# Performance work log

Hardware: AMD Instinct MI355X
Metric: run time of the kernel (lower is better)

## Reference

```python
import jax, jax.numpy as jnp
import numpy as np

SEQLEN = 4096
DIM = 4096
HIDDEN = 11008  # multiple_of=256 rounding of int(2*16384/3)


def setup_inputs() -> dict:
    key = jax.random.key(0)
    k1, k2, k3, k4 = jax.random.split(key, 4)
    scale = 1.0 / np.sqrt(DIM)
    return {
        "x": jax.random.normal(k1, (SEQLEN, DIM), dtype=jnp.float32),
        "weight_1": jax.random.normal(k2, (DIM, HIDDEN), dtype=jnp.float32) * scale,
        "weight_2": jax.random.normal(k3, (HIDDEN, DIM), dtype=jnp.float32) * (1.0 / np.sqrt(HIDDEN)),
        "weight_3": jax.random.normal(k4, (DIM, HIDDEN), dtype=jnp.float32) * scale,
    }


def reference(x, weight_1, weight_2, weight_3):
    # The torch module decomposes these GEMMs into 128x128 tile loops, but
    # the math is exactly the standard SwiGLU FFN:
    #   out = (silu(x @ W1) * (x @ W3)) @ W2
    gate = x @ weight_1                      # [S, H]
    up = x @ weight_3                        # [S, H]
    h = jax.nn.silu(gate) * up               # [S, H]
    return h @ weight_2                      # [S, D]
```

## Files before the change

kernel.cpp:

```cpp
#include <hip/hip_runtime.h>
#include <stdint.h>
#include <stddef.h>

#define AS1 __attribute__((address_space(1)))
#define AS3 __attribute__((address_space(3)))

typedef __attribute__((ext_vector_type(8))) short bf16x8;
typedef __attribute__((ext_vector_type(4))) float f32x4;

static constexpr int S = 4096, D = 4096, HID = 11008;

__device__ __forceinline__ unsigned short f2bf(float f) {
  unsigned u = __float_as_uint(f);
  u += 0x7FFFu + ((u >> 16) & 1u);
  return (unsigned short)(u >> 16);
}

__device__ __forceinline__ void async16(const void* gsrc, void* ldst) {
  __builtin_amdgcn_global_load_lds((AS1 void*)const_cast<void*>(gsrc),
                                   (AS3 void*)ldst, 16, 0, 0);
}

__global__ __launch_bounds__(256) void k_cvt_bf16(const float* __restrict__ src,
                                                  unsigned short* __restrict__ dst) {
  int i = blockIdx.x * 256 + threadIdx.x;
  const float4* s = (const float4*)src;
  float4 a = s[2 * i];
  float4 b = s[2 * i + 1];
  union { unsigned short h[8]; uint4 v; } r;
  r.h[0] = f2bf(a.x); r.h[1] = f2bf(a.y); r.h[2] = f2bf(a.z); r.h[3] = f2bf(a.w);
  r.h[4] = f2bf(b.x); r.h[5] = f2bf(b.y); r.h[6] = f2bf(b.z); r.h[7] = f2bf(b.w);
  ((uint4*)dst)[i] = r.v;
}

__global__ __launch_bounds__(256) void k_tcvt(const float* __restrict__ src,
                                              unsigned short* __restrict__ dst,
                                              int R, int C) {
  __shared__ float tile[64][65];
  const int tid = threadIdx.x;
  const int c0 = blockIdx.x * 64;
  const int r0 = blockIdx.y * 64;
#pragma unroll
  for (int it = 0; it < 16; ++it) {
    int f = it * 256 + tid;
    int r = f >> 6, c = f & 63;
    tile[r][c] = src[(size_t)(r0 + r) * C + (c0 + c)];
  }
  __syncthreads();
#pragma unroll
  for (int it = 0; it < 8; ++it) {
    int f = it * 512 + tid * 2;
    int cc = f >> 6, rr = f & 63;
    unsigned p0 = f2bf(tile[rr][cc]);
    unsigned p1 = f2bf(tile[rr + 1][cc]);
    *(unsigned*)(dst + (size_t)(c0 + cc) * R + (r0 + rr)) = p0 | (p1 << 16);
  }
}

__global__ __launch_bounds__(256, 2) void gemm_gateup(
    const unsigned short* __restrict__ A,
    const unsigned short* __restrict__ B1,
    const unsigned short* __restrict__ B3,
    unsigned short* __restrict__ Hout) {
  __shared__ __align__(16) unsigned short sA[128 * 32];
  __shared__ __align__(16) unsigned short sB1[64 * 32];
  __shared__ __align__(16) unsigned short sB3[64 * 32];

  const int tid = threadIdx.x;
  const int wave = tid >> 6, lane = tid & 63;
  const int wy = wave >> 1, wx = wave & 1;
  const int lm = lane & 15, lq = lane >> 4;
  const int m0 = blockIdx.x * 128;
  const int n0 = blockIdx.y * 64;

  const int ci0 = wave * 64 + lane;
  const int rA0 = ci0 >> 2, cA0 = (ci0 & 3) * 8;
  const int ci1 = ci0 + 256;
  const int rA1 = ci1 >> 2, cA1 = (ci1 & 3) * 8;

  const unsigned short* pA0 = A + (size_t)(m0 + rA0) * D + cA0;
  const unsigned short* pA1 = A + (size_t)(m0 + rA1) * D + cA1;
  const unsigned short* pB1 = B1 + (size_t)(n0 + rA0) * D + cA0;
  const unsigned short* pB3 = B3 + (size_t)(n0 + rA0) * D + cA0;
  unsigned short* lA0 = sA + wave * 512;
  unsigned short* lA1 = sA + 2048 + wave * 512;
  unsigned short* lB1 = sB1 + wave * 512;
  unsigned short* lB3 = sB3 + wave * 512;

  f32x4 zero = {0.f, 0.f, 0.f, 0.f};
  f32x4 accg[4][2], accu[4][2];
#pragma unroll
  for (int i = 0; i < 4; ++i)
#pragma unroll
    for (int j = 0; j < 2; ++j) { accg[i][j] = zero; accu[i][j] = zero; }

  for (int kt = 0; kt < D / 32; ++kt) {
    __syncthreads();
    async16(pA0, lA0);
    async16(pA1, lA1);
    async16(pB1, lB1);
    async16(pB3, lB3);
    pA0 += 32; pA1 += 32; pB1 += 32; pB3 += 32;
    __syncthreads();

    bf16x8 af[4];
#pragma unroll
    for (int i = 0; i < 4; ++i)
      af[i] = *(const bf16x8*)(sA + (wy * 64 + i * 16 + lm) * 32 + lq * 8);
#pragma unroll
    for (int j = 0; j < 2; ++j) {
      bf16x8 b1f = *(const bf16x8*)(sB1 + (wx * 32 + j * 16 + lm) * 32 + lq * 8);
      bf16x8 b3f = *(const bf16x8*)(sB3 + (wx * 32 + j * 16 + lm) * 32 + lq * 8);
#pragma unroll
      for (int i = 0; i < 4; ++i) {
        accg[i][j] = __builtin_amdgcn_mfma_f32_16x16x32_bf16(af[i], b1f, accg[i][j], 0, 0, 0);
        accu[i][j] = __builtin_amdgcn_mfma_f32_16x16x32_bf16(af[i], b3f, accu[i][j], 0, 0, 0);
      }
    }
  }

#pragma unroll
  for (int i = 0; i < 4; ++i)
#pragma unroll
    for (int j = 0; j < 2; ++j) {
      int col = n0 + wx * 32 + j * 16 + lm;
#pragma unroll
      for (int r = 0; r < 4; ++r) {
        int row = m0 + wy * 64 + i * 16 + lq * 4 + r;
        float g = accg[i][j][r];
        float u = accu[i][j][r];
        float hv = (g / (1.0f + __expf(-g))) * u;
        Hout[(size_t)row * HID + col] = f2bf(hv);
      }
    }
}

__global__ __launch_bounds__(256, 2) void gemm_out(
    const unsigned short* __restrict__ A,
    const unsigned short* __restrict__ B,
    float* __restrict__ C) {
  __shared__ __align__(16) unsigned short sA[128 * 32];
  __shared__ __align__(16) unsigned short sB[128 * 32];

  const int tid = threadIdx.x;
  const int wave = tid >> 6, lane = tid & 63;
  const int wy = wave >> 1, wx = wave & 1;
  const int lm = lane & 15, lq = lane >> 4;
  const int m0 = blockIdx.x * 128;
  const int n0 = blockIdx.y * 128;

  const int ci0 = wave * 64 + lane;
  const int r0 = ci0 >> 2, c0 = (ci0 & 3) * 8;
  const int ci1 = ci0 + 256;
  const int r1 = ci1 >> 2, c1 = (ci1 & 3) * 8;

  const unsigned short* pA0 = A + (size_t)(m0 + r0) * HID + c0;
  const unsigned short* pA1 = A + (size_t)(m0 + r1) * HID + c1;
  const unsigned short* pB0 = B + (size_t)(n0 + r0) * HID + c0;
  const unsigned short* pB1 = B + (size_t)(n0 + r1) * HID + c1;
  unsigned short* lA0 = sA + wave * 512;
  unsigned short* lA1 = sA + 2048 + wave * 512;
  unsigned short* lB0 = sB + wave * 512;
  unsigned short* lB1 = sB + 2048 + wave * 512;

  f32x4 zero = {0.f, 0.f, 0.f, 0.f};
  f32x4 acc[4][4];
#pragma unroll
  for (int i = 0; i < 4; ++i)
#pragma unroll
    for (int j = 0; j < 4; ++j) acc[i][j] = zero;

  for (int kt = 0; kt < HID / 32; ++kt) {
    __syncthreads();
    async16(pA0, lA0);
    async16(pA1, lA1);
    async16(pB0, lB0);
    async16(pB1, lB1);
    pA0 += 32; pA1 += 32; pB0 += 32; pB1 += 32;
    __syncthreads();

    bf16x8 af[4];
#pragma unroll
    for (int i = 0; i < 4; ++i)
      af[i] = *(const bf16x8*)(sA + (wy * 64 + i * 16 + lm) * 32 + lq * 8);
#pragma unroll
    for (int j = 0; j < 4; ++j) {
      bf16x8 bfj = *(const bf16x8*)(sB + (wx * 64 + j * 16 + lm) * 32 + lq * 8);
#pragma unroll
      for (int i = 0; i < 4; ++i)
        acc[i][j] = __builtin_amdgcn_mfma_f32_16x16x32_bf16(af[i], bfj, acc[i][j], 0, 0, 0);
    }
  }

#pragma unroll
  for (int i = 0; i < 4; ++i)
#pragma unroll
    for (int j = 0; j < 4; ++j) {
      int col = n0 + wx * 64 + j * 16 + lm;
#pragma unroll
      for (int r = 0; r < 4; ++r) {
        int row = m0 + wy * 64 + i * 16 + lq * 4 + r;
        C[(size_t)row * D + col] = acc[i][j][r];
      }
    }
}

extern "C" void kernel_launch(void* const* d_in, const int* in_sizes, int n_in,
                              void* d_out, int out_size, void* d_ws, size_t ws_size,
                              hipStream_t stream) {
  const float* x  = (const float*)d_in[0];
  const float* w1 = (const float*)d_in[1];
  const float* w2 = (const float*)d_in[2];
  const float* w3 = (const float*)d_in[3];
  float* out = (float*)d_out;

  char* ws = (char*)d_ws;
  unsigned short* xb   = (unsigned short*)(ws);
  unsigned short* w1t  = (unsigned short*)(ws + (size_t)33554432);
  unsigned short* w3t  = (unsigned short*)(ws + (size_t)123731968);
  unsigned short* hbuf = (unsigned short*)(ws + (size_t)213909504);
  unsigned short* w2t  = w1t;

  k_cvt_bf16<<<dim3((S * D) / 8 / 256), 256, 0, stream>>>(x, xb);
  k_tcvt<<<dim3(HID / 64, D / 64), 256, 0, stream>>>(w1, w1t, D, HID);
  k_tcvt<<<dim3(HID / 64, D / 64), 256, 0, stream>>>(w3, w3t, D, HID);
  gemm_gateup<<<dim3(S / 128, HID / 64), 256, 0, stream>>>(xb, w1t, w3t, hbuf);
  k_tcvt<<<dim3(D / 64, HID / 64), 256, 0, stream>>>(w2, w2t, HID, D);
  gemm_out<<<dim3(S / 128, D / 128), 256, 0, stream>>>(hbuf, w2t, out);
}
```

Measured before the change: 1.822 ms.

## Rewrite both GEMMs with larger tiles, 4-stage async LDS pipeline and swizzle

Both GEMM kernels move to 512-thread blocks with 256x128 (gate/up) and 256x256 (out) tiles. A 4-deep ring of global-to-LDS async loads is driven by explicit vmcnt waits and split barriers. The LDS layout is XOR-swizzled to avoid bank conflicts, and block indices are remapped across XCDs. MFMA phases get raised wave priority. The aim is to hide global load latency and raise arithmetic intensity, at the cost of 128KB LDS per block and heavy register pressure from the larger accumulator sets.

```diff
diff --git a/kernel.cpp b/kernel.cpp
--- a/kernel.cpp
+++ b/kernel.cpp
@@ -57,76 +57,124 @@
   }
 }
 
-__global__ __launch_bounds__(256, 2) void gemm_gateup(
+
+__global__ __launch_bounds__(512, 2) void gemm_gateup(
     const unsigned short* __restrict__ A,
     const unsigned short* __restrict__ B1,
     const unsigned short* __restrict__ B3,
     unsigned short* __restrict__ Hout) {
-  __shared__ __align__(16) unsigned short sA[128 * 32];
-  __shared__ __align__(16) unsigned short sB1[64 * 32];
-  __shared__ __align__(16) unsigned short sB3[64 * 32];
-
+  __shared__ __align__(16) unsigned short sL[65536];
+  constexpr int NT = D / 32;
   const int tid = threadIdx.x;
   const int wave = tid >> 6, lane = tid & 63;
-  const int wy = wave >> 1, wx = wave & 1;
+  const int wy = wave >> 2, wx = wave & 3;
   const int lm = lane & 15, lq = lane >> 4;
-  const int m0 = blockIdx.x * 128;
-  const int n0 = blockIdx.y * 64;
-
-  const int ci0 = wave * 64 + lane;
-  const int rA0 = ci0 >> 2, cA0 = (ci0 & 3) * 8;
-  const int ci1 = ci0 + 256;
-  const int rA1 = ci1 >> 2, cA1 = (ci1 & 3) * 8;
-
-  const unsigned short* pA0 = A + (size_t)(m0 + rA0) * D + cA0;
-  const unsigned short* pA1 = A + (size_t)(m0 + rA1) * D + cA1;
-  const unsigned short* pB1 = B1 + (size_t)(n0 + rA0) * D + cA0;
-  const unsigned short* pB3 = B3 + (size_t)(n0 + rA0) * D + cA0;
-  unsigned short* lA0 = sA + wave * 512;
-  unsigned short* lA1 = sA + 2048 + wave * 512;
-  unsigned short* lB1 = sB1 + wave * 512;
-  unsigned short* lB3 = sB3 + wave * 512;
+
+  const int q = (int)gridDim.x >> 3;
+  const int wg = (blockIdx.x & 7) * q + (blockIdx.x >> 3);
+  const int m0 = (wg / (HID / 128)) * 256;
+  const int n0 = (wg % (HID / 128)) * 128;
+
+  const int h = lm >> 1;
+  const int sw = ((((lm & 1) << 2) | lq) ^ h);
+  const int aBase  = (wy * 64 + h) * 64 + sw * 8;
+  const int b1Base = 8192  + (wx * 16 + h) * 64 + sw * 8;
+  const int b3Base = 12288 + (wx * 16 + h) * 64 + sw * 8;
+
+  const int p0 = tid >> 3, s0 = tid & 7;
+  const int u0 = s0 ^ (p0 & 7);
+  const int rr0 = 2 * p0 + (u0 >> 2);
+  const int kc0 = (u0 & 3) * 8;
+
+  const unsigned short* pA0 = A  + (size_t)(m0 + rr0) * D + kc0;
+  const unsigned short* pA1 = pA0 + (size_t)128 * D;
+  const unsigned short* pB1 = B1 + (size_t)(n0 + rr0) * D + kc0;
+  const unsigned short* pB3 = B3 + (size_t)(n0 + rr0) * D + kc0;
 
   f32x4 zero = {0.f, 0.f, 0.f, 0.f};
-  f32x4 accg[4][2], accu[4][2];
-#pragma unroll
-  for (int i = 0; i < 4; ++i)
+  f32x4 accg[8][2], accu[8][2];
+#pragma unroll
+  for (int i = 0; i < 8; ++i)
 #pragma unroll
     for (int j = 0; j < 2; ++j) { accg[i][j] = zero; accu[i][j] = zero; }
 
-  for (int kt = 0; kt < D / 32; ++kt) {
-    __syncthreads();
-    async16(pA0, lA0);
-    async16(pA1, lA1);
-    async16(pB1, lB1);
-    async16(pB3, lB3);
+#pragma unroll
+  for (int x = 0; x < 3; ++x) {
+    const int nso = x * 16384;
+    async16(pA0, sL + nso + wave * 512);
+    async16(pA1, sL + nso + 4096 + wave * 512);
+    async16(pB1, sL + nso + 8192 + wave * 512);
+    async16(pB3, sL + nso + 12288 + wave * 512);
     pA0 += 32; pA1 += 32; pB1 += 32; pB3 += 32;
-    __syncthreads();
-
-    bf16x8 af[4];
+  }
+  asm volatile("s_waitcnt vmcnt(8)" ::: "memory");
+  __builtin_amdgcn_s_barrier();
+
+  for (int t = 0; t < NT; ++t) {
+    const int so  = (t & 3) * 16384;
+    const int nso = ((t + 3) & 3) * 16384;
+    const bool st = (t + 3 < NT);
+    bf16x8 b1f[2], b3f[2], af[4];
+#pragma unroll
+    for (int j = 0; j < 2; ++j) {
+      b1f[j] = *(const bf16x8*)(sL + so + b1Base + j * 512);
+      b3f[j] = *(const bf16x8*)(sL + so + b3Base + j * 512);
+    }
 #pragma unroll
     for (int i = 0; i < 4; ++i)
-      af[i] = *(const bf16x8*)(sA + (wy * 64 + i * 16 + lm) * 32 + lq * 8);
+      af[i] = *(const bf16x8*)(sL + so + aBase + i * 512);
+    if (st) {
+      async16(pA0, sL + nso + wave * 512);
+      async16(pA1, sL + nso + 4096 + wave * 512);
+      pA0 += 32; pA1 += 32;
+    }
+    __builtin_amdgcn_s_barrier();
+    asm volatile("s_waitcnt lgkmcnt(0)" ::: "memory");
+    __builtin_amdgcn_sched_barrier(0);
+    __builtin_amdgcn_s_setprio(1);
+#pragma unroll
+    for (int j = 0; j < 2; ++j)
+#pragma unroll
+      for (int i = 0; i < 4; ++i) {
+        accg[i][j] = __builtin_amdgcn_mfma_f32_16x16x32_bf16(af[i], b1f[j], accg[i][j], 0, 0, 0);
+        accu[i][j] = __builtin_amdgcn_mfma_f32_16x16x32_bf16(af[i], b3f[j], accu[i][j], 0, 0, 0);
+      }
+    __builtin_amdgcn_s_setprio(0);
+    __builtin_amdgcn_s_barrier();
+#pragma unroll
+    for (int i = 0; i < 4; ++i)
+      af[i] = *(const bf16x8*)(sL + so + aBase + (4 + i) * 512);
+    if (st) {
+      async16(pB1, sL + nso + 8192 + wave * 512);
+      async16(pB3, sL + nso + 12288 + wave * 512);
+      pB1 += 32; pB3 += 32;
+    }
+    __builtin_amdgcn_s_barrier();
+    asm volatile("s_waitcnt lgkmcnt(0)" ::: "memory");
+    __builtin_amdgcn_sched_barrier(0);
+    __builtin_amdgcn_s_setprio(1);
+#pragma unroll
+    for (int j = 0; j < 2; ++j)
+#pragma unroll
+      for (int i = 0; i < 4; ++i) {
+        accg[4 + i][j] = __builtin_amdgcn_mfma_f32_16x16x32_bf16(af[i], b1f[j], accg[4 + i][j], 0, 0, 0);
+        accu[4 + i][j] = __builtin_amdgcn_mfma_f32_16x16x32_bf16(af[i], b3f[j], accu[4 + i][j], 0, 0, 0);
+      }
+    __builtin_amdgcn_s_setprio(0);
+    if (t + 3 < NT)      asm volatile("s_waitcnt vmcnt(8)" ::: "memory");
+    else if (t + 2 < NT) asm volatile("s_waitcnt vmcnt(4)" ::: "memory");
+    else if (t + 1 < NT) asm volatile("s_waitcnt vmcnt(0)" ::: "memory");
+    __builtin_amdgcn_s_barrier();
+  }
+
+#pragma unroll
+  for (int i = 0; i < 8; ++i)
 #pragma unroll
     for (int j = 0; j < 2; ++j) {
-      bf16x8 b1f = *(const bf16x8*)(sB1 + (wx * 32 + j * 16 + lm) * 32 + lq * 8);
-      bf16x8 b3f = *(const bf16x8*)(sB3 + (wx * 32 + j * 16 + lm) * 32 + lq * 8);
-#pragma unroll
-      for (int i = 0; i < 4; ++i) {
-        accg[i][j] = __builtin_amdgcn_mfma_f32_16x16x32_bf16(af[i], b1f, accg[i][j], 0, 0, 0);
-        accu[i][j] = __builtin_amdgcn_mfma_f32_16x16x32_bf16(af[i], b3f, accu[i][j], 0, 0, 0);
-      }
-    }
-  }
-
-#pragma unroll
-  for (int i = 0; i < 4; ++i)
-#pragma unroll
-    for (int j = 0; j < 2; ++j) {
-      int col = n0 + wx * 32 + j * 16 + lm;
+      const int col = n0 + wx * 32 + j * 16 + lm;
 #pragma unroll
       for (int r = 0; r < 4; ++r) {
-        int row = m0 + wy * 64 + i * 16 + lq * 4 + r;
+        const int row = m0 + wy * 128 + i * 16 + lq * 4 + r;
         float g = accg[i][j][r];
         float u = accu[i][j][r];
         float hv = (g / (1.0f + __expf(-g))) * u;
@@ -135,71 +183,115 @@
     }
 }
 
-__global__ __launch_bounds__(256, 2) void gemm_out(
+__global__ __launch_bounds__(512, 2) void gemm_out(
     const unsigned short* __restrict__ A,
     const unsigned short* __restrict__ B,
     float* __restrict__ C) {
-  __shared__ __align__(16) unsigned short sA[128 * 32];
-  __shared__ __align__(16) unsigned short sB[128 * 32];
-
+  __shared__ __align__(16) unsigned short sL[65536];
+  constexpr int NT = HID / 32;
   const int tid = threadIdx.x;
   const int wave = tid >> 6, lane = tid & 63;
-  const int wy = wave >> 1, wx = wave & 1;
+  const int wy = wave >> 2, wx = wave & 3;
   const int lm = lane & 15, lq = lane >> 4;
-  const int m0 = blockIdx.x * 128;
-  const int n0 = blockIdx.y * 128;
-
-  const int ci0 = wave * 64 + lane;
-  const int r0 = ci0 >> 2, c0 = (ci0 & 3) * 8;
-  const int ci1 = ci0 + 256;
-  const int r1 = ci1 >> 2, c1 = (ci1 & 3) * 8;
-
-  const unsigned short* pA0 = A + (size_t)(m0 + r0) * HID + c0;
-  const unsigned short* pA1 = A + (size_t)(m0 + r1) * HID + c1;
-  const unsigned short* pB0 = B + (size_t)(n0 + r0) * HID + c0;
-  const unsigned short* pB1 = B + (size_t)(n0 + r1) * HID + c1;
-  unsigned short* lA0 = sA + wave * 512;
-  unsigned short* lA1 = sA + 2048 + wave * 512;
-  unsigned short* lB0 = sB + wave * 512;
-  unsigned short* lB1 = sB + 2048 + wave * 512;
+
+  const int q = (int)gridDim.x >> 3;
+  const int wg = (blockIdx.x & 7) * q + (blockIdx.x >> 3);
+  const int m0 = (wg >> 4) * 256;
+  const int n0 = (wg & 15) * 256;
+
+  const int h = lm >> 1;
+  const int sw = ((((lm & 1) << 2) | lq) ^ h);
+  const int aBase = (wy * 64 + h) * 64 + sw * 8;
+  const int bBase = 8192 + (wx * 32 + h) * 64 + sw * 8;
+
+  const int p0 = tid >> 3, s0 = tid & 7;
+  const int u0 = s0 ^ (p0 & 7);
+  const int rr0 = 2 * p0 + (u0 >> 2);
+  const int kc0 = (u0 & 3) * 8;
+
+  const unsigned short* pA0 = A + (size_t)(m0 + rr0) * HID + kc0;
+  const unsigned short* pA1 = pA0 + (size_t)128 * HID;
+  const unsigned short* pB0 = B + (size_t)(n0 + rr0) * HID + kc0;
+  const unsigned short* pB1 = pB0 + (size_t)128 * HID;
 
   f32x4 zero = {0.f, 0.f, 0.f, 0.f};
-  f32x4 acc[4][4];
-#pragma unroll
-  for (int i = 0; i < 4; ++i)
+  f32x4 acc[8][4];
+#pragma unroll
+  for (int i = 0; i < 8; ++i)
 #pragma unroll
     for (int j = 0; j < 4; ++j) acc[i][j] = zero;
 
-  for (int kt = 0; kt < HID / 32; ++kt) {
-    __syncthreads();
-    async16(pA0, lA0);
-    async16(pA1, lA1);
-    async16(pB0, lB0);
-    async16(pB1, lB1);
+#pragma unroll
+  for (int x = 0; x < 3; ++x) {
+    const int nso = x * 16384;
+    async16(pA0, sL + nso + wave * 512);
+    async16(pA1, sL + nso + 4096 + wave * 512);
+    async16(pB0, sL + nso + 8192 + wave * 512);
+    async16(pB1, sL + nso + 12288 + wave * 512);
     pA0 += 32; pA1 += 32; pB0 += 32; pB1 += 32;
-    __syncthreads();
-
-    bf16x8 af[4];
+  }
+  asm volatile("s_waitcnt vmcnt(8)" ::: "memory");
+  __builtin_amdgcn_s_barrier();
+
+  for (int t = 0; t < NT; ++t) {
+    const int so  = (t & 3) * 16384;
+    const int nso = ((t + 3) & 3) * 16384;
+    const bool st = (t + 3 < NT);
+    bf16x8 bf[4], af[4];
+#pragma unroll
+    for (int j = 0; j < 4; ++j)
+      bf[j] = *(const bf16x8*)(sL + so + bBase + j * 512);
 #pragma unroll
     for (int i = 0; i < 4; ++i)
-      af[i] = *(const bf16x8*)(sA + (wy * 64 + i * 16 + lm) * 32 + lq * 8);
+      af[i] = *(const bf16x8*)(sL + so + aBase + i * 512);
+    if (st) {
+      async16(pA0, sL + nso + wave * 512);
+      async16(pA1, sL + nso + 4096 + wave * 512);
+      pA0 += 32; pA1 += 32;
+    }
+    __builtin_amdgcn_s_barrier();
+    asm volatile("s_waitcnt lgkmcnt(0)" ::: "memory");
+    __builtin_amdgcn_sched_barrier(0);
+    __builtin_amdgcn_s_setprio(1);
+#pragma unroll
+    for (int j = 0; j < 4; ++j)
+#pragma unroll
+      for (int i = 0; i < 4; ++i)
+        acc[i][j] = __builtin_amdgcn_mfma_f32_16x16x32_bf16(af[i], bf[j], acc[i][j], 0, 0, 0);
+    __builtin_amdgcn_s_setprio(0);
+    __builtin_amdgcn_s_barrier();
+#pragma unroll
+    for (int i = 0; i < 4; ++i)
+      af[i] = *(const bf16x8*)(sL + so + aBase + (4 + i) * 512);
+    if (st) {
+      async16(pB0, sL + nso + 8192 + wave * 512);
+      async16(pB1, sL + nso + 12288 + wave * 512);
+      pB0 += 32; pB1 += 32;
+    }
+    __builtin_amdgcn_s_barrier();
+    asm volatile("s_waitcnt lgkmcnt(0)" ::: "memory");
+    __builtin_amdgcn_sched_barrier(0);
+    __builtin_amdgcn_s_setprio(1);
+#pragma unroll
+    for (int j = 0; j < 4; ++j)
+#pragma unroll
+      for (int i = 0; i < 4; ++i)
+        acc[4 + i][j] = __builtin_amdgcn_mfma_f32_16x16x32_bf16(af[i], bf[j], acc[4 + i][j], 0, 0, 0);
+    __builtin_amdgcn_s_setprio(0);
+    if (t + 3 < NT)      asm volatile("s_waitcnt vmcnt(8)" ::: "memory");
+    else if (t + 2 < NT) asm volatile("s_waitcnt vmcnt(4)" ::: "memory");
+    else if (t + 1 < NT) asm volatile("s_waitcnt vmcnt(0)" ::: "memory");
+    __builtin_amdgcn_s_barrier();
+  }
+
+#pragma unroll
+  for (int i = 0; i < 8; ++i)
 #pragma unroll
     for (int j = 0; j < 4; ++j) {
-      bf16x8 bfj = *(const bf16x8*)(sB + (wx * 64 + j * 16 + lm) * 32 + lq * 8);
-#pragma unroll
-      for (int i = 0; i < 4; ++i)
-        acc[i][j] = __builtin_amdgcn_mfma_f32_16x16x32_bf16(af[i], bfj, acc[i][j], 0, 0, 0);
-    }
-  }
-
-#pragma unroll
-  for (int i = 0; i < 4; ++i)
-#pragma unroll
-    for (int j = 0; j < 4; ++j) {
-      int col = n0 + wx * 64 + j * 16 + lm;
+      const int col = n0 + wx * 64 + j * 16 + lm;
 #pragma unroll
       for (int r = 0; r < 4; ++r) {
-        int row = m0 + wy * 64 + i * 16 + lq * 4 + r;
+        const int row = m0 + wy * 128 + i * 16 + lq * 4 + r;
         C[(size_t)row * D + col] = acc[i][j][r];
       }
     }
@@ -224,7 +316,7 @@
   k_cvt_bf16<<<dim3((S * D) / 8 / 256), 256, 0, stream>>>(x, xb);
   k_tcvt<<<dim3(HID / 64, D / 64), 256, 0, stream>>>(w1, w1t, D, HID);
   k_tcvt<<<dim3(HID / 64, D / 64), 256, 0, stream>>>(w3, w3t, D, HID);
-  gemm_gateup<<<dim3(S / 128, HID / 64), 256, 0, stream>>>(xb, w1t, w3t, hbuf);
+  gemm_gateup<<<dim3((S / 256) * (HID / 128)), 512, 0, stream>>>(xb, w1t, w3t, hbuf);
   k_tcvt<<<dim3(D / 64, HID / 64), 256, 0, stream>>>(w2, w2t, HID, D);
-  gemm_out<<<dim3(S / 128, D / 128), 256, 0, stream>>>(hbuf, w2t, out);
-}
+  gemm_out<<<dim3((S / 256) * (D / 256)), 512, 0, stream>>>(hbuf, w2t, out);
+}
```

Result: faster. 1.563 ms (-14.2%).
